# Kernel optimization log

Hardware: AMD Instinct MI355X
Metric: run time of the kernel (lower is better)

## Reference

```python
import jax, jax.numpy as jnp
import numpy as np

# weight_dict {0:1,1:1,2:1,3:1} with similarity_pyramid=True -> w_l = 1/2^l
WEIGHTS = [1.0, 0.5, 0.25, 0.125]
WINS = [9, 9, 7, 5]
NCC_FACTOR = 100.0
N_LOSSES = 2  # ['mse', 'ncc']


def _sliding_sum(x, win, axis):
    """Box (ones-kernel) sliding-window sum along one axis, 'same' output via
    zero padding of win//2 on each side -- separable equivalent of the dense
    ones-kernel conv in the original NCC_loss."""
    pad = win // 2
    pw = [(0, 0)] * x.ndim
    pw[axis] = (pad + 1, pad)  # extra leading zero so cumsum diff gives window sums
    c = jnp.cumsum(jnp.pad(x, pw), axis=axis)
    n = x.shape[axis]
    hi = jax.lax.slice_in_dim(c, win, win + n, axis=axis)
    lo = jax.lax.slice_in_dim(c, 0, n, axis=axis)
    return hi - lo


def _box_sum(x, win):
    # x: [B,1,H,W]; 2D box filter == separable 1D sliding sums
    return _sliding_sum(_sliding_sum(x, win, 2), win, 3)


def _ncc_loss(y_pred, y_true, win):
    Ii, Ji = y_true, y_pred
    ws = float(win * win)
    I_sum = _box_sum(Ii, win)
    J_sum = _box_sum(Ji, win)
    I2_sum = _box_sum(Ii * Ii, win)
    J2_sum = _box_sum(Ji * Ji, win)
    IJ_sum = _box_sum(Ii * Ji, win)
    u_I = I_sum / ws
    u_J = J_sum / ws
    cross = IJ_sum - u_J * I_sum - u_I * J_sum + u_I * u_J * ws
    I_var = I2_sum - 2.0 * u_I * I_sum + u_I * u_I * ws
    J_var = J2_sum - 2.0 * u_J * J_sum + u_J * u_J * ws
    cc = cross * cross / (I_var * J_var + 1e-8)
    return -jnp.sum(jnp.mean(cc, axis=0)) / NCC_FACTOR


def _l2_loss(inp, tgt):
    # sum over spatial dims, mean over batch & channel
    return jnp.mean(jnp.sum((inp - tgt) ** 2, axis=(2, 3)))


def _hier_loss(y_hats, y):
    total = jnp.zeros((), dtype=y.dtype)
    levels = []
    for l, yh in enumerate(y_hats):
        if yh.shape == y.shape:
            yt = y
        else:
            # F.interpolate bilinear align_corners=False == half-pixel linear resize
            yt = jax.image.resize(y, yh.shape, method='linear', antialias=False)
        w = WEIGHTS[l]
        ll = (w * _l2_loss(yh, yt) + w * _ncc_loss(yh, yt, WINS[l])) / N_LOSSES
        levels.append(ll)
        total = total + ll
    return total, levels


def setup_inputs() -> dict:
    key = jax.random.key(0)
    ks = jax.random.split(key, 5)
    return {
        'y_hat_0': jax.random.uniform(ks[0], (32, 1, 512, 512), dtype=jnp.float32),
        'y_hat_1': jax.random.uniform(ks[1], (32, 1, 256, 256), dtype=jnp.float32),
        'y_hat_2': jax.random.uniform(ks[2], (32, 1, 128, 128), dtype=jnp.float32),
        'y_hat_3': jax.random.uniform(ks[3], (32, 1, 64, 64), dtype=jnp.float32),
        'y': jax.random.uniform(ks[4], (32, 1, 512, 512), dtype=jnp.float32),
    }


def reference(y_hat_0, y_hat_1, y_hat_2, y_hat_3, y):
    total, levels = _hier_loss([y_hat_0, y_hat_1, y_hat_2, y_hat_3], y)
    return (total, *levels)
```

## Files before the change

### kernel.cpp

```cpp
#include <hip/hip_runtime.h>

#define NT 256
#define RCHUNK 32
#define NSLOT 32


__device__ __forceinline__ void wave_fence_after_write() {
    __builtin_amdgcn_wave_barrier();
    asm volatile("s_waitcnt lgkmcnt(0)" ::: "memory");
    __builtin_amdgcn_sched_barrier(0);
}
__device__ __forceinline__ void wave_fence_after_read() {
    __builtin_amdgcn_wave_barrier();
    __builtin_amdgcn_sched_barrier(0);
}

template<int W, int H, int WIN, int SCALE>
__device__ void level_wave(const float* __restrict__ yh,
                           const float* __restrict__ y,
                           int sub, float* __restrict__ ws_acc, int level,
                           float* rawI, float* rawJ)
{
    constexpr int HW = WIN / 2;
    constexpr int RW = 64 + 2 * HW;
    constexpr int T  = RCHUNK + 2 * HW;
    constexpr int G  = (T + WIN - 1) / WIN;
    constexpr float INV_WS = 1.0f / (float)(WIN * WIN);

    constexpr int STRIPS = W / 64;
    constexpr int CHUNKS = H / RCHUNK;
    int b     = sub / (STRIPS * CHUNKS);
    int rem   = sub % (STRIPS * CHUNKS);
    int chunk = rem / STRIPS;
    int strip = rem % STRIPS;
    int r0 = chunk * RCHUNK;
    int c0 = strip * 64;

    const float* Jimg = yh + (size_t)b * W * H;
    const float* Yimg = y  + (size_t)b * 512 * 512;

    int l = threadIdx.x & 63;

    float ringI[WIN], ringJ[WIN], ringII[WIN], ringJJ[WIN], ringIJ[WIN];
#pragma unroll
    for (int k = 0; k < WIN; ++k) {
        ringI[k] = 0.f; ringJ[k] = 0.f; ringII[k] = 0.f; ringJJ[k] = 0.f; ringIJ[k] = 0.f;
    }
    float vI = 0.f, vJ = 0.f, vII = 0.f, vJJ = 0.f, vIJ = 0.f;
    float l2acc = 0.f, ccacc = 0.f;

    for (int g = 0; g < G; ++g) {
#pragma unroll
        for (int u = 0; u < WIN; ++u) {
            int rr = g * WIN + u;
            int r  = r0 - HW + rr;
            bool rin = (rr < T) && (r >= 0) && (r < H);

            {
                int j = c0 - HW + l;
                float I = 0.f, J = 0.f;
                if (rin && j >= 0 && j < W) {
                    J = Jimg[(size_t)r * W + j];
                    if (SCALE == 1) {
                        I = Yimg[(size_t)r * 512 + j];
                    } else {
                        constexpr int OFF = (SCALE - 2) / 2;
                        const float* p = Yimg + (size_t)(SCALE * r + OFF) * 512 + (SCALE * j + OFF);
                        I = 0.25f * (p[0] + p[1] + p[512] + p[513]);
                    }
                }
                rawI[l] = I;
                rawJ[l] = J;
                if (l < RW - 64) {
                    int j2 = j + 64;
                    float I2 = 0.f, J2 = 0.f;
                    if (rin && j2 < W) {
                        J2 = Jimg[(size_t)r * W + j2];
                        if (SCALE == 1) {
                            I2 = Yimg[(size_t)r * 512 + j2];
                        } else {
                            constexpr int OFF = (SCALE - 2) / 2;
                            const float* p = Yimg + (size_t)(SCALE * r + OFF) * 512 + (SCALE * j2 + OFF);
                            I2 = 0.25f * (p[0] + p[1] + p[512] + p[513]);
                        }
                    }
                    rawI[l + 64] = I2;
                    rawJ[l + 64] = J2;
                }
            }
            wave_fence_after_write();

            float sI = 0.f, sJ = 0.f, sII = 0.f, sJJ = 0.f, sIJ = 0.f;
            float Ic = 0.f, Jc = 0.f;
#pragma unroll
            for (int k = 0; k < WIN; ++k) {
                float I = rawI[l + k];
                float J = rawJ[l + k];
                if (k == HW) { Ic = I; Jc = J; }
                sI += I; sJ += J;
                sII = fmaf(I, I, sII);
                sJJ = fmaf(J, J, sJJ);
                sIJ = fmaf(I, J, sIJ);
            }
            wave_fence_after_read();

            if (rr >= HW && rr < RCHUNK + HW) {
                float d = Jc - Ic;
                l2acc = fmaf(d, d, l2acc);
            }

            ringI[u] = sI; ringJ[u] = sJ; ringII[u] = sII; ringJJ[u] = sJJ; ringIJ[u] = sIJ;
            vI += sI; vJ += sJ; vII += sII; vJJ += sJJ; vIJ += sIJ;

            if (rr >= 2 * HW && rr < T) {
                float cross = fmaf(-(vI * vJ), INV_WS, vIJ);
                float Iv    = fmaf(-(vI * vI), INV_WS, vII);
                float Jv    = fmaf(-(vJ * vJ), INV_WS, vJJ);
                float cc = (cross * cross) / (Iv * Jv + 1e-8f);
                ccacc += cc;
                constexpr int dummy = 0; (void)dummy;
                const int us = (u + 1) % WIN;
                vI  -= ringI[us];
                vJ  -= ringJ[us];
                vII -= ringII[us];
                vJJ -= ringJJ[us];
                vIJ -= ringIJ[us];
            }
        }
    }

#pragma unroll
    for (int off = 32; off > 0; off >>= 1) {
        l2acc += __shfl_down(l2acc, off);
        ccacc += __shfl_down(ccacc, off);
    }
    if (l == 0) {
        int slot = sub & (NSLOT - 1);
        atomicAdd(&ws_acc[(level * 2 + 0) * NSLOT + slot], l2acc);
        atomicAdd(&ws_acc[(level * 2 + 1) * NSLOT + slot], ccacc);
    }
}

__global__ __launch_bounds__(NT)
void hier_loss_kernel(const float* __restrict__ yh0, const float* __restrict__ yh1,
                      const float* __restrict__ yh2, const float* __restrict__ yh3,
                      const float* __restrict__ y, float* ws_acc)
{
    __shared__ float smem[4][2][80];
    int wave = threadIdx.x >> 6;
    float* rawI = &smem[wave][0][0];
    float* rawJ = &smem[wave][1][0];

    int wid = blockIdx.x * (NT / 64) + wave;
    if (wid < 4096) {
        level_wave<512, 512, 9, 1>(yh0, y, wid, ws_acc, 0, rawI, rawJ);
    } else if (wid < 5120) {
        level_wave<256, 256, 9, 2>(yh1, y, wid - 4096, ws_acc, 1, rawI, rawJ);
    } else if (wid < 5376) {
        level_wave<128, 128, 7, 4>(yh2, y, wid - 5120, ws_acc, 2, rawI, rawJ);
    } else {
        level_wave<64, 64, 5, 8>(yh3, y, wid - 5376, ws_acc, 3, rawI, rawJ);
    }
}

__global__ void hier_finalize_kernel(const float* __restrict__ ws_acc, float* __restrict__ out)
{
    if (threadIdx.x == 0 && blockIdx.x == 0) {
        const float wts[4] = {1.0f, 0.5f, 0.25f, 0.125f};
        float total = 0.f;
#pragma unroll
        for (int lv = 0; lv < 4; ++lv) {
            float l2s = 0.f, ccs = 0.f;
            for (int s = 0; s < NSLOT; ++s) {
                l2s += ws_acc[(lv * 2 + 0) * NSLOT + s];
                ccs += ws_acc[(lv * 2 + 1) * NSLOT + s];
            }
            float l2  = l2s / 32.0f;
            float ncc = -ccs / (32.0f * 100.0f);
            float ll  = wts[lv] * (l2 + ncc) * 0.5f;
            out[1 + lv] = ll;
            total += ll;
        }
        out[0] = total;
    }
}

extern "C" void kernel_launch(void* const* d_in, const int* in_sizes, int n_in,
                              void* d_out, int out_size, void* d_ws, size_t ws_size,
                              hipStream_t stream)
{
    const float* yh0 = (const float*)d_in[0];
    const float* yh1 = (const float*)d_in[1];
    const float* yh2 = (const float*)d_in[2];
    const float* yh3 = (const float*)d_in[3];
    const float* y   = (const float*)d_in[4];
    float* ws_acc = (float*)d_ws;
    float* out = (float*)d_out;

    hipMemsetAsync(ws_acc, 0, 8 * NSLOT * sizeof(float), stream);
    hier_loss_kernel<<<5440 / (NT / 64), NT, 0, stream>>>(yh0, yh1, yh2, yh3, y, ws_acc);
    hier_finalize_kernel<<<1, 64, 0, stream>>>(ws_acc, out);
}
```

Measured before the change: 121.9 us.

## Process two columns per lane with vector buffer loads instead of LDS staging

Each lane now computes two adjacent output columns over 128-wide strips, so half as many waves are launched. Horizontal window sums are formed in registers from overlapping 128-bit buffer loads, which replaces the per-row LDS staging and wave fences. Buffer descriptors with a record count of zero for invalid rows handle padding through hardware out-of-bounds zeroing. The NCC divide becomes a fast reciprocal, and the horizontal sums for the two columns share their interior terms; this costs more registers and extra redundant loaded bytes per lane, and the 64-wide level now maps onto a 128-column strip.

```diff
diff --git a/kernel.cpp b/kernel.cpp
--- a/kernel.cpp
+++ b/kernel.cpp
@@ -4,49 +4,72 @@
 #define RCHUNK 32
 #define NSLOT 32
 
-
-__device__ __forceinline__ void wave_fence_after_write() {
-    __builtin_amdgcn_wave_barrier();
-    asm volatile("s_waitcnt lgkmcnt(0)" ::: "memory");
-    __builtin_amdgcn_sched_barrier(0);
-}
-__device__ __forceinline__ void wave_fence_after_read() {
-    __builtin_amdgcn_wave_barrier();
-    __builtin_amdgcn_sched_barrier(0);
-}
-
-template<int W, int H, int WIN, int SCALE>
-__device__ void level_wave(const float* __restrict__ yh,
-                           const float* __restrict__ y,
-                           int sub, float* __restrict__ ws_acc, int level,
-                           float* rawI, float* rawJ)
+typedef float f4 __attribute__((ext_vector_type(4)));
+
+__device__ __forceinline__ f4 bl4(__amdgpu_buffer_rsrc_t r, int voff) {
+    auto d = __builtin_amdgcn_raw_buffer_load_b128(r, voff, 0, 0);
+    return __builtin_bit_cast(f4, d);
+}
+
+__device__ __forceinline__ float ccval(float sI, float sJ, float sII, float sJJ,
+                                       float sIJ, float inv_ws) {
+    float cross = fmaf(-(sI * sJ), inv_ws, sIJ);
+    float iv    = fmaf(-(sI * sI), inv_ws, sII);
+    float jv    = fmaf(-(sJ * sJ), inv_ws, sJJ);
+    float den   = fmaf(iv, jv, 1e-8f);
+    return (cross * cross) * __builtin_amdgcn_rcpf(den);
+}
+
+template<int W, int H, int WIN, int S>
+__device__ __forceinline__ void level_wave(const float* __restrict__ yh,
+                                           const float* __restrict__ y,
+                                           int sub, float* __restrict__ ws_acc,
+                                           int level)
 {
     constexpr int HW = WIN / 2;
-    constexpr int RW = 64 + 2 * HW;
     constexpr int T  = RCHUNK + 2 * HW;
     constexpr int G  = (T + WIN - 1) / WIN;
+    constexpr int SE = (-HW) & 3;
+    constexpr int SO = (2 - HW) & 3;
+    constexpr int SMAX = SE > SO ? SE : SO;
+    constexpr int NF4J = (WIN + 1 + SMAX + 3) / 4;
+    constexpr int OFF = (S - 2) / 2;
+    constexpr int SHI = (S <= 2) ? 0 : (OFF & 3);
+    constexpr int NF4I = (S == 1) ? NF4J : (S * WIN + SHI + 2 + 3) / 4;
     constexpr float INV_WS = 1.0f / (float)(WIN * WIN);
 
-    constexpr int STRIPS = W / 64;
+    constexpr int STRIPS = (W + 127) / 128;
     constexpr int CHUNKS = H / RCHUNK;
+
     int b     = sub / (STRIPS * CHUNKS);
-    int rem   = sub % (STRIPS * CHUNKS);
+    int rem   = sub - b * (STRIPS * CHUNKS);
     int chunk = rem / STRIPS;
-    int strip = rem % STRIPS;
-    int r0 = chunk * RCHUNK;
-    int c0 = strip * 64;
-
-    const float* Jimg = yh + (size_t)b * W * H;
-    const float* Yimg = y  + (size_t)b * 512 * 512;
+    int strip = rem - chunk * STRIPS;
+
+    int r0 = __builtin_amdgcn_readfirstlane(chunk * RCHUNK);
+    int bu = __builtin_amdgcn_readfirstlane(b);
+    const float* Jb = yh + (size_t)bu * (W * H);
+    const float* Yb = y  + (size_t)bu * (512 * 512);
 
     int l = threadIdx.x & 63;
-
-    float ringI[WIN], ringJ[WIN], ringII[WIN], ringJJ[WIN], ringIJ[WIN];
+    bool odd = (l & 1) != 0;
+    int c0 = strip * 128;
+    int ub = c0 + 2 * l - HW;
+    int voffJ = (ub & ~3) * 4;
+    int voffI;
+    if constexpr (S == 1) voffI = voffJ;
+    else                  voffI = ((S * ub + OFF) & ~3) * 4;
+
+    float rIA[WIN], rIB[WIN], rJA[WIN], rJB[WIN], rIIA[WIN], rIIB[WIN],
+          rJJA[WIN], rJJB[WIN], rIJA[WIN], rIJB[WIN];
 #pragma unroll
     for (int k = 0; k < WIN; ++k) {
-        ringI[k] = 0.f; ringJ[k] = 0.f; ringII[k] = 0.f; ringJJ[k] = 0.f; ringIJ[k] = 0.f;
-    }
-    float vI = 0.f, vJ = 0.f, vII = 0.f, vJJ = 0.f, vIJ = 0.f;
+        rIA[k] = 0.f; rIB[k] = 0.f; rJA[k] = 0.f; rJB[k] = 0.f;
+        rIIA[k] = 0.f; rIIB[k] = 0.f; rJJA[k] = 0.f; rJJB[k] = 0.f;
+        rIJA[k] = 0.f; rIJB[k] = 0.f;
+    }
+    float vIA=0.f, vIB=0.f, vJA=0.f, vJB=0.f, vIIA=0.f, vIIB=0.f,
+          vJJA=0.f, vJJB=0.f, vIJA=0.f, vIJB=0.f;
     float l2acc = 0.f, ccacc = 0.f;
 
     for (int g = 0; g < G; ++g) {
@@ -54,77 +77,103 @@
         for (int u = 0; u < WIN; ++u) {
             int rr = g * WIN + u;
             int r  = r0 - HW + rr;
-            bool rin = (rr < T) && (r >= 0) && (r < H);
-
+            bool valid = (r >= 0) && (r < H) && (rr < T);
+            int nrecJ = valid ? W * 4 : 0;
+            int nrecY = valid ? 512 * 4 : 0;
+
+            float qJ[WIN + 1], qI[WIN + 1];
             {
-                int j = c0 - HW + l;
-                float I = 0.f, J = 0.f;
-                if (rin && j >= 0 && j < W) {
-                    J = Jimg[(size_t)r * W + j];
-                    if (SCALE == 1) {
-                        I = Yimg[(size_t)r * 512 + j];
-                    } else {
-                        constexpr int OFF = (SCALE - 2) / 2;
-                        const float* p = Yimg + (size_t)(SCALE * r + OFF) * 512 + (SCALE * j + OFF);
-                        I = 0.25f * (p[0] + p[1] + p[512] + p[513]);
+                auto rJ = __builtin_amdgcn_make_buffer_rsrc(
+                    (void*)(Jb + (long)r * W), (short)0, nrecJ, 0x00020000);
+                float LJ[NF4J * 4];
+#pragma unroll
+                for (int k = 0; k < NF4J; ++k) {
+                    f4 v = bl4(rJ, voffJ + 16 * k);
+                    LJ[4*k+0] = v.x; LJ[4*k+1] = v.y; LJ[4*k+2] = v.z; LJ[4*k+3] = v.w;
+                }
+#pragma unroll
+                for (int e = 0; e <= WIN; ++e)
+                    qJ[e] = odd ? LJ[e + SO] : LJ[e + SE];
+            }
+            if constexpr (S == 1) {
+                auto rI = __builtin_amdgcn_make_buffer_rsrc(
+                    (void*)(Yb + (long)r * 512), (short)0, nrecY, 0x00020000);
+                float LI[NF4J * 4];
+#pragma unroll
+                for (int k = 0; k < NF4J; ++k) {
+                    f4 v = bl4(rI, voffI + 16 * k);
+                    LI[4*k+0] = v.x; LI[4*k+1] = v.y; LI[4*k+2] = v.z; LI[4*k+3] = v.w;
+                }
+#pragma unroll
+                for (int e = 0; e <= WIN; ++e)
+                    qI[e] = odd ? LI[e + SO] : LI[e + SE];
+            } else {
+                int yr = S * r + OFF;
+                float p[WIN + 1];
+                {
+                    auto rA = __builtin_amdgcn_make_buffer_rsrc(
+                        (void*)(Yb + (long)yr * 512), (short)0, nrecY, 0x00020000);
+                    float LA[NF4I * 4];
+#pragma unroll
+                    for (int k = 0; k < NF4I; ++k) {
+                        f4 v = bl4(rA, voffI + 16 * k);
+                        LA[4*k+0] = v.x; LA[4*k+1] = v.y; LA[4*k+2] = v.z; LA[4*k+3] = v.w;
                     }
-                }
-                rawI[l] = I;
-                rawJ[l] = J;
-                if (l < RW - 64) {
-                    int j2 = j + 64;
-                    float I2 = 0.f, J2 = 0.f;
-                    if (rin && j2 < W) {
-                        J2 = Jimg[(size_t)r * W + j2];
-                        if (SCALE == 1) {
-                            I2 = Yimg[(size_t)r * 512 + j2];
-                        } else {
-                            constexpr int OFF = (SCALE - 2) / 2;
-                            const float* p = Yimg + (size_t)(SCALE * r + OFF) * 512 + (SCALE * j2 + OFF);
-                            I2 = 0.25f * (p[0] + p[1] + p[512] + p[513]);
-                        }
+#pragma unroll
+                    for (int e = 0; e <= WIN; ++e)
+                        p[e] = LA[S*e + SHI] + LA[S*e + SHI + 1];
+                }
+                {
+                    auto rB = __builtin_amdgcn_make_buffer_rsrc(
+                        (void*)(Yb + (long)(yr + 1) * 512), (short)0, nrecY, 0x00020000);
+                    float LB[NF4I * 4];
+#pragma unroll
+                    for (int k = 0; k < NF4I; ++k) {
+                        f4 v = bl4(rB, voffI + 16 * k);
+                        LB[4*k+0] = v.x; LB[4*k+1] = v.y; LB[4*k+2] = v.z; LB[4*k+3] = v.w;
                     }
-                    rawI[l + 64] = I2;
-                    rawJ[l + 64] = J2;
-                }
-            }
-            wave_fence_after_write();
-
-            float sI = 0.f, sJ = 0.f, sII = 0.f, sJJ = 0.f, sIJ = 0.f;
-            float Ic = 0.f, Jc = 0.f;
-#pragma unroll
-            for (int k = 0; k < WIN; ++k) {
-                float I = rawI[l + k];
-                float J = rawJ[l + k];
-                if (k == HW) { Ic = I; Jc = J; }
-                sI += I; sJ += J;
-                sII = fmaf(I, I, sII);
-                sJJ = fmaf(J, J, sJJ);
-                sIJ = fmaf(I, J, sIJ);
-            }
-            wave_fence_after_read();
-
-            if (rr >= HW && rr < RCHUNK + HW) {
-                float d = Jc - Ic;
-                l2acc = fmaf(d, d, l2acc);
-            }
-
-            ringI[u] = sI; ringJ[u] = sJ; ringII[u] = sII; ringJJ[u] = sJJ; ringIJ[u] = sIJ;
-            vI += sI; vJ += sJ; vII += sII; vJJ += sJJ; vIJ += sIJ;
-
+#pragma unroll
+                    for (int e = 0; e <= WIN; ++e)
+                        p[e] += LB[S*e + SHI] + LB[S*e + SHI + 1];
+                }
+#pragma unroll
+                for (int e = 0; e <= WIN; ++e)
+                    qI[e] = 0.25f * p[e];
+            }
+
+            float mI=0.f, mJ=0.f, mII=0.f, mJJ=0.f, mIJ=0.f;
+#pragma unroll
+            for (int e = 1; e < WIN; ++e) {
+                mI += qI[e]; mJ += qJ[e];
+                mII = fmaf(qI[e], qI[e], mII);
+                mJJ = fmaf(qJ[e], qJ[e], mJJ);
+                mIJ = fmaf(qI[e], qJ[e], mIJ);
+            }
+            float hIA = mI + qI[0],  hIB = mI + qI[WIN];
+            float hJA = mJ + qJ[0],  hJB = mJ + qJ[WIN];
+            float hIIA = fmaf(qI[0], qI[0], mII), hIIB = fmaf(qI[WIN], qI[WIN], mII);
+            float hJJA = fmaf(qJ[0], qJ[0], mJJ), hJJB = fmaf(qJ[WIN], qJ[WIN], mJJ);
+            float hIJA = fmaf(qI[0], qJ[0], mIJ), hIJB = fmaf(qI[WIN], qJ[WIN], mIJ);
+
+            rIA[u]=hIA; rIB[u]=hIB; rJA[u]=hJA; rJB[u]=hJB;
+            rIIA[u]=hIIA; rIIB[u]=hIIB; rJJA[u]=hJJA; rJJB[u]=hJJB;
+            rIJA[u]=hIJA; rIJB[u]=hIJB;
+            vIA+=hIA; vIB+=hIB; vJA+=hJA; vJB+=hJB; vIIA+=hIIA; vIIB+=hIIB;
+            vJJA+=hJJA; vJJB+=hJJB; vIJA+=hIJA; vIJB+=hIJB;
+
+            if (rr >= HW && rr < HW + RCHUNK) {
+                float dA = qJ[HW] - qI[HW];
+                float dB = qJ[HW + 1] - qI[HW + 1];
+                l2acc = fmaf(dA, dA, l2acc);
+                l2acc = fmaf(dB, dB, l2acc);
+            }
             if (rr >= 2 * HW && rr < T) {
-                float cross = fmaf(-(vI * vJ), INV_WS, vIJ);
-                float Iv    = fmaf(-(vI * vI), INV_WS, vII);
-                float Jv    = fmaf(-(vJ * vJ), INV_WS, vJJ);
-                float cc = (cross * cross) / (Iv * Jv + 1e-8f);
-                ccacc += cc;
-                constexpr int dummy = 0; (void)dummy;
-                const int us = (u + 1) % WIN;
-                vI  -= ringI[us];
-                vJ  -= ringJ[us];
-                vII -= ringII[us];
-                vJJ -= ringJJ[us];
-                vIJ -= ringIJ[us];
+                ccacc += ccval(vIA, vJA, vIIA, vJJA, vIJA, INV_WS);
+                ccacc += ccval(vIB, vJB, vIIB, vJJB, vIJB, INV_WS);
+                const int uo = (u + 1) % WIN;
+                vIA-=rIA[uo]; vIB-=rIB[uo]; vJA-=rJA[uo]; vJB-=rJB[uo];
+                vIIA-=rIIA[uo]; vIIB-=rIIB[uo]; vJJA-=rJJA[uo]; vJJB-=rJJB[uo];
+                vIJA-=rIJA[uo]; vIJB-=rIJB[uo];
             }
         }
     }
@@ -146,20 +195,15 @@
                       const float* __restrict__ yh2, const float* __restrict__ yh3,
                       const float* __restrict__ y, float* ws_acc)
 {
-    __shared__ float smem[4][2][80];
-    int wave = threadIdx.x >> 6;
-    float* rawI = &smem[wave][0][0];
-    float* rawJ = &smem[wave][1][0];
-
-    int wid = blockIdx.x * (NT / 64) + wave;
-    if (wid < 4096) {
-        level_wave<512, 512, 9, 1>(yh0, y, wid, ws_acc, 0, rawI, rawJ);
-    } else if (wid < 5120) {
-        level_wave<256, 256, 9, 2>(yh1, y, wid - 4096, ws_acc, 1, rawI, rawJ);
-    } else if (wid < 5376) {
-        level_wave<128, 128, 7, 4>(yh2, y, wid - 5120, ws_acc, 2, rawI, rawJ);
+    int wid = blockIdx.x * (NT / 64) + (threadIdx.x >> 6);
+    if (wid < 2048) {
+        level_wave<512, 512, 9, 1>(yh0, y, wid, ws_acc, 0);
+    } else if (wid < 2560) {
+        level_wave<256, 256, 9, 2>(yh1, y, wid - 2048, ws_acc, 1);
+    } else if (wid < 2688) {
+        level_wave<128, 128, 7, 4>(yh2, y, wid - 2560, ws_acc, 2);
     } else {
-        level_wave<64, 64, 5, 8>(yh3, y, wid - 5376, ws_acc, 3, rawI, rawJ);
+        level_wave<64, 64, 5, 8>(yh3, y, wid - 2688, ws_acc, 3);
     }
 }
 
@@ -198,6 +242,6 @@
     float* out = (float*)d_out;
 
     hipMemsetAsync(ws_acc, 0, 8 * NSLOT * sizeof(float), stream);
-    hier_loss_kernel<<<5440 / (NT / 64), NT, 0, stream>>>(yh0, yh1, yh2, yh3, y, ws_acc);
+    hier_loss_kernel<<<2752 / (NT / 64), NT, 0, stream>>>(yh0, yh1, yh2, yh3, y, ws_acc);
     hier_finalize_kernel<<<1, 64, 0, stream>>>(ws_acc, out);
 }
```

Result: slower. 219.8 us (+80.3%).

## Process wider column strips per block with double-buffered shared rows and prefetch

Applied to the files above, without the earlier changes.

Each block now handles a strip of up to 256 columns instead of each wave handling 64, which cuts the redundant halo loads at strip edges. Shared-memory rows are double-buffered and the next row is prefetched into registers before the barrier, so global loads overlap with the sliding-window arithmetic. The division is replaced by a hardware reciprocal. The cost is a block-wide __syncthreads per row instead of wave-local fences, and idle threads on the smaller levels (only 128 or 64 of 256 threads compute).

```diff
diff --git a/kernel.cpp b/kernel.cpp
--- a/kernel.cpp
+++ b/kernel.cpp
@@ -3,128 +3,120 @@
 #define NT 256
 #define RCHUNK 32
 #define NSLOT 32
+#define RWMAX (NT + 8)
 
-
-__device__ __forceinline__ void wave_fence_after_write() {
-    __builtin_amdgcn_wave_barrier();
-    asm volatile("s_waitcnt lgkmcnt(0)" ::: "memory");
-    __builtin_amdgcn_sched_barrier(0);
-}
-__device__ __forceinline__ void wave_fence_after_read() {
-    __builtin_amdgcn_wave_barrier();
-    __builtin_amdgcn_sched_barrier(0);
+__device__ __forceinline__ float ccval(float sI, float sJ, float sII, float sJJ,
+                                       float sIJ, float inv_ws) {
+    float cross = fmaf(-(sI * sJ), inv_ws, sIJ);
+    float iv    = fmaf(-(sI * sI), inv_ws, sII);
+    float jv    = fmaf(-(sJ * sJ), inv_ws, sJJ);
+    float den   = fmaf(iv, jv, 1e-8f);
+    return (cross * cross) * __builtin_amdgcn_rcpf(den);
 }
 
-template<int W, int H, int WIN, int SCALE>
-__device__ void level_wave(const float* __restrict__ yh,
-                           const float* __restrict__ y,
-                           int sub, float* __restrict__ ws_acc, int level,
-                           float* rawI, float* rawJ)
+struct St { float J, i0, i1, i2, i3; };
+
+template<int W, int H, int WIN, int S, int CW>
+__device__ __forceinline__ void level_block(const float* __restrict__ yh,
+                                            const float* __restrict__ y,
+                                            int sub, float* __restrict__ ws_acc,
+                                            int level,
+                                            float (*bufI)[RWMAX], float (*bufJ)[RWMAX])
 {
-    constexpr int HW = WIN / 2;
-    constexpr int RW = 64 + 2 * HW;
-    constexpr int T  = RCHUNK + 2 * HW;
-    constexpr int G  = (T + WIN - 1) / WIN;
+    constexpr int HW  = WIN / 2;
+    constexpr int RW  = CW + 2 * HW;
+    constexpr int T   = RCHUNK + 2 * HW;
+    constexpr int G   = (T + WIN - 1) / WIN;
+    constexpr int NIT = G * WIN;
+    constexpr int OFF = (S - 2) / 2;
+    constexpr int WRAP = RW - NT;
     constexpr float INV_WS = 1.0f / (float)(WIN * WIN);
 
-    constexpr int STRIPS = W / 64;
+    constexpr int STRIPS = W / CW;
     constexpr int CHUNKS = H / RCHUNK;
+
     int b     = sub / (STRIPS * CHUNKS);
-    int rem   = sub % (STRIPS * CHUNKS);
+    int rem   = sub - b * (STRIPS * CHUNKS);
     int chunk = rem / STRIPS;
-    int strip = rem % STRIPS;
+    int strip = rem - chunk * STRIPS;
     int r0 = chunk * RCHUNK;
-    int c0 = strip * 64;
+    int c0 = strip * CW;
 
-    const float* Jimg = yh + (size_t)b * W * H;
-    const float* Yimg = y  + (size_t)b * 512 * 512;
+    const float* Jb = yh + (size_t)b * (W * H);
+    const float* Yb = y  + (size_t)b * (512 * 512);
 
-    int l = threadIdx.x & 63;
+    int t  = threadIdx.x;
+    int jA = c0 - HW + t;
+    int jB = jA + NT;
 
-    float ringI[WIN], ringJ[WIN], ringII[WIN], ringJJ[WIN], ringIJ[WIN];
+    auto fetch = [&](int rr, int j, St& s) {
+        s.J = 0.f; s.i0 = 0.f; s.i1 = 0.f; s.i2 = 0.f; s.i3 = 0.f;
+        int r = r0 - HW + rr;
+        if (rr < NIT && r >= 0 && r < H && j >= 0 && j < W) {
+            s.J = Jb[(size_t)r * W + j];
+            if constexpr (S == 1) {
+                s.i0 = Yb[(size_t)r * 512 + j];
+            } else {
+                int yr = S * r + OFF;
+                const float* p = Yb + (size_t)yr * 512 + (S * j + OFF);
+                s.i0 = p[0]; s.i1 = p[1]; s.i2 = p[512]; s.i3 = p[513];
+            }
+        }
+    };
+    auto ival = [&](const St& s) -> float {
+        if constexpr (S == 1) return s.i0;
+        else return 0.25f * ((s.i0 + s.i1) + (s.i2 + s.i3));
+    };
+
+    float rI[WIN], rJ[WIN], rII[WIN], rJJ[WIN], rIJ[WIN];
 #pragma unroll
-    for (int k = 0; k < WIN; ++k) {
-        ringI[k] = 0.f; ringJ[k] = 0.f; ringII[k] = 0.f; ringJJ[k] = 0.f; ringIJ[k] = 0.f;
-    }
-    float vI = 0.f, vJ = 0.f, vII = 0.f, vJJ = 0.f, vIJ = 0.f;
+    for (int k = 0; k < WIN; ++k) { rI[k]=0.f; rJ[k]=0.f; rII[k]=0.f; rJJ[k]=0.f; rIJ[k]=0.f; }
+    float vI=0.f, vJ=0.f, vII=0.f, vJJ=0.f, vIJ=0.f;
     float l2acc = 0.f, ccacc = 0.f;
+
+    St sA, sB;
+    fetch(0, jA, sA);
+    sB.J = 0.f; sB.i0 = 0.f; sB.i1 = 0.f; sB.i2 = 0.f; sB.i3 = 0.f;
+    if constexpr (WRAP > 0) { if (t < WRAP) fetch(0, jB, sB); }
 
     for (int g = 0; g < G; ++g) {
 #pragma unroll
         for (int u = 0; u < WIN; ++u) {
             int rr = g * WIN + u;
-            int r  = r0 - HW + rr;
-            bool rin = (rr < T) && (r >= 0) && (r < H);
+            float* bI = bufI[rr & 1];
+            float* bJ = bufJ[rr & 1];
 
-            {
-                int j = c0 - HW + l;
-                float I = 0.f, J = 0.f;
-                if (rin && j >= 0 && j < W) {
-                    J = Jimg[(size_t)r * W + j];
-                    if (SCALE == 1) {
-                        I = Yimg[(size_t)r * 512 + j];
-                    } else {
-                        constexpr int OFF = (SCALE - 2) / 2;
-                        const float* p = Yimg + (size_t)(SCALE * r + OFF) * 512 + (SCALE * j + OFF);
-                        I = 0.25f * (p[0] + p[1] + p[512] + p[513]);
-                    }
+            bI[t] = ival(sA);
+            bJ[t] = sA.J;
+            if constexpr (WRAP > 0) {
+                if (t < WRAP) { bI[t + NT] = ival(sB); bJ[t + NT] = sB.J; }
+            }
+            fetch(rr + 1, jA, sA);
+            if constexpr (WRAP > 0) { if (t < WRAP) fetch(rr + 1, jB, sB); }
+            __syncthreads();
+            if (t < CW) {
+                float sIs=0.f, sJs=0.f, sIIs=0.f, sJJs=0.f, sIJs=0.f, Ic=0.f, Jc=0.f;
+#pragma unroll
+                for (int k = 0; k < WIN; ++k) {
+                    float I = bI[t + k];
+                    float J = bJ[t + k];
+                    if (k == HW) { Ic = I; Jc = J; }
+                    sIs += I; sJs += J;
+                    sIIs = fmaf(I, I, sIIs);
+                    sJJs = fmaf(J, J, sJJs);
+                    sIJs = fmaf(I, J, sIJs);
                 }
-                rawI[l] = I;
-                rawJ[l] = J;
-                if (l < RW - 64) {
-                    int j2 = j + 64;
-                    float I2 = 0.f, J2 = 0.f;
-                    if (rin && j2 < W) {
-                        J2 = Jimg[(size_t)r * W + j2];
-                        if (SCALE == 1) {
-                            I2 = Yimg[(size_t)r * 512 + j2];
-                        } else {
-                            constexpr int OFF = (SCALE - 2) / 2;
-                            const float* p = Yimg + (size_t)(SCALE * r + OFF) * 512 + (SCALE * j2 + OFF);
-                            I2 = 0.25f * (p[0] + p[1] + p[512] + p[513]);
-                        }
-                    }
-                    rawI[l + 64] = I2;
-                    rawJ[l + 64] = J2;
+                if (rr >= HW && rr < HW + RCHUNK) {
+                    float d = Jc - Ic;
+                    l2acc = fmaf(d, d, l2acc);
                 }
-            }
-            wave_fence_after_write();
-
-            float sI = 0.f, sJ = 0.f, sII = 0.f, sJJ = 0.f, sIJ = 0.f;
-            float Ic = 0.f, Jc = 0.f;
-#pragma unroll
-            for (int k = 0; k < WIN; ++k) {
-                float I = rawI[l + k];
-                float J = rawJ[l + k];
-                if (k == HW) { Ic = I; Jc = J; }
-                sI += I; sJ += J;
-                sII = fmaf(I, I, sII);
-                sJJ = fmaf(J, J, sJJ);
-                sIJ = fmaf(I, J, sIJ);
-            }
-            wave_fence_after_read();
-
-            if (rr >= HW && rr < RCHUNK + HW) {
-                float d = Jc - Ic;
-                l2acc = fmaf(d, d, l2acc);
-            }
-
-            ringI[u] = sI; ringJ[u] = sJ; ringII[u] = sII; ringJJ[u] = sJJ; ringIJ[u] = sIJ;
-            vI += sI; vJ += sJ; vII += sII; vJJ += sJJ; vIJ += sIJ;
-
-            if (rr >= 2 * HW && rr < T) {
-                float cross = fmaf(-(vI * vJ), INV_WS, vIJ);
-                float Iv    = fmaf(-(vI * vI), INV_WS, vII);
-                float Jv    = fmaf(-(vJ * vJ), INV_WS, vJJ);
-                float cc = (cross * cross) / (Iv * Jv + 1e-8f);
-                ccacc += cc;
-                constexpr int dummy = 0; (void)dummy;
-                const int us = (u + 1) % WIN;
-                vI  -= ringI[us];
-                vJ  -= ringJ[us];
-                vII -= ringII[us];
-                vJJ -= ringJJ[us];
-                vIJ -= ringIJ[us];
+                rI[u]=sIs; rJ[u]=sJs; rII[u]=sIIs; rJJ[u]=sJJs; rIJ[u]=sIJs;
+                vI+=sIs; vJ+=sJs; vII+=sIIs; vJJ+=sJJs; vIJ+=sIJs;
+                if (rr >= 2 * HW && rr < T) {
+                    ccacc += ccval(vI, vJ, vII, vJJ, vIJ, INV_WS);
+                    const int uo = (u + 1) % WIN;
+                    vI-=rI[uo]; vJ-=rJ[uo]; vII-=rII[uo]; vJJ-=rJJ[uo]; vIJ-=rIJ[uo];
+                }
             }
         }
     }
@@ -134,8 +126,9 @@
         l2acc += __shfl_down(l2acc, off);
         ccacc += __shfl_down(ccacc, off);
     }
-    if (l == 0) {
-        int slot = sub & (NSLOT - 1);
+    int lane = t & 63;
+    if (lane == 0) {
+        int slot = (blockIdx.x * 4 + (t >> 6)) & (NSLOT - 1);
         atomicAdd(&ws_acc[(level * 2 + 0) * NSLOT + slot], l2acc);
         atomicAdd(&ws_acc[(level * 2 + 1) * NSLOT + slot], ccacc);
     }
@@ -146,20 +139,17 @@
                       const float* __restrict__ yh2, const float* __restrict__ yh3,
                       const float* __restrict__ y, float* ws_acc)
 {
-    __shared__ float smem[4][2][80];
-    int wave = threadIdx.x >> 6;
-    float* rawI = &smem[wave][0][0];
-    float* rawJ = &smem[wave][1][0];
-
-    int wid = blockIdx.x * (NT / 64) + wave;
-    if (wid < 4096) {
-        level_wave<512, 512, 9, 1>(yh0, y, wid, ws_acc, 0, rawI, rawJ);
-    } else if (wid < 5120) {
-        level_wave<256, 256, 9, 2>(yh1, y, wid - 4096, ws_acc, 1, rawI, rawJ);
-    } else if (wid < 5376) {
-        level_wave<128, 128, 7, 4>(yh2, y, wid - 5120, ws_acc, 2, rawI, rawJ);
+    __shared__ float bufI[2][RWMAX];
+    __shared__ float bufJ[2][RWMAX];
+    int bid = blockIdx.x;
+    if (bid < 1024) {
+        level_block<512, 512, 9, 1, 256>(yh0, y, bid, ws_acc, 0, bufI, bufJ);
+    } else if (bid < 1280) {
+        level_block<256, 256, 9, 2, 256>(yh1, y, bid - 1024, ws_acc, 1, bufI, bufJ);
+    } else if (bid < 1408) {
+        level_block<128, 128, 7, 4, 128>(yh2, y, bid - 1280, ws_acc, 2, bufI, bufJ);
     } else {
-        level_wave<64, 64, 5, 8>(yh3, y, wid - 5376, ws_acc, 3, rawI, rawJ);
+        level_block<64, 64, 5, 8, 64>(yh3, y, bid - 1408, ws_acc, 3, bufI, bufJ);
     }
 }
 
@@ -198,6 +188,6 @@
     float* out = (float*)d_out;
 
     hipMemsetAsync(ws_acc, 0, 8 * NSLOT * sizeof(float), stream);
-    hier_loss_kernel<<<5440 / (NT / 64), NT, 0, stream>>>(yh0, yh1, yh2, yh3, y, ws_acc);
+    hier_loss_kernel<<<1472, NT, 0, stream>>>(yh0, yh1, yh2, yh3, y, ws_acc);
     hier_finalize_kernel<<<1, 64, 0, stream>>>(ws_acc, out);
 }
```

After: 106.2 us. 1.15x faster.
